# Kernel optimization log

Measured on AMD Instinct MI355X. Metric: run time of the kernel, lower is better.

Reference implementation:

```python
import jax, jax.numpy as jnp
import numpy as np

WS = 8          # window size
DISP = 4        # ws // 2 cyclic shift displacement
WS2 = WS * WS   # tokens per window
HEADS = 3
HD = 32         # head dim
SCALE = HD ** -0.5


def _mask(upper_lower, left_right):
    m = np.zeros((WS2, WS2), np.float32)
    if upper_lower:
        m[-DISP * WS:, :-DISP * WS] = -np.inf
        m[:-DISP * WS, -DISP * WS:] = -np.inf
    if left_right:
        m = m.reshape(WS, WS, WS, WS)
        m[:, -DISP:, :, :-DISP] = -np.inf
        m[:, :-DISP, :, -DISP:] = -np.inf
        m = m.reshape(WS2, WS2)
    return m

UL = _mask(True, False)
LR = _mask(False, True)
_ix = np.array([(i, j) for i in range(WS) for j in range(WS)])
REL = (_ix[None] - _ix[:, None]) + WS - 1  # [WS2, WS2, 2] relative index table


def _ln(x, g, b):
    m = x.mean(-1, keepdims=True)
    v = ((x - m) ** 2).mean(-1, keepdims=True)
    return (x - m) * jax.lax.rsqrt(v + 1e-5) * g + b


def _wattn(x, Wqkv, pos, Wo, bo, shifted):
    if shifted:
        x = jnp.roll(x, (-DISP, -DISP), axis=(1, 2))
    b, H, W, _ = x.shape
    nh, nw = H // WS, W // WS
    # qkv: last dim laid out as (3, heads, head_dim) matching torch chunk + rearrange
    qkv = (x @ Wqkv).reshape(b, nh, WS, nw, WS, 3, HEADS, HD)
    qkv = qkv.transpose(5, 0, 6, 1, 3, 2, 4, 7).reshape(3, b, HEADS, nh * nw, WS2, HD)
    q, k, v = qkv[0], qkv[1], qkv[2]
    dots = jnp.einsum('bhwid,bhwjd->bhwij', q, k) * SCALE  # [b,h,nwin,ws2,ws2]
    dots = dots + pos[REL[..., 0], REL[..., 1]]            # relative pos bias
    if shifted:
        m = np.zeros((nh * nw, WS2, WS2), np.float32)
        m[-nw:] += UL             # windows in last row
        m[nw - 1::nw] += LR       # windows in last column
        dots = dots + jnp.asarray(m)[None, None]
    a = jax.nn.softmax(dots, axis=-1)
    o = jnp.einsum('bhwij,bhwjd->bhwid', a, v)
    o = o.reshape(b, HEADS, nh, nw, WS, WS, HD).transpose(0, 2, 4, 3, 5, 1, 6).reshape(b, H, W, HEADS * HD)
    o = o @ Wo + bo
    if shifted:
        o = jnp.roll(o, (DISP, DISP), axis=(1, 2))
    return o


def _block(t, g1, b1, Wqkv, pos, Wo, bo, g2, b2, W1, bf1, W2, bf2, shifted):
    t = t + _wattn(_ln(t, g1, b1), Wqkv, pos, Wo, bo, shifted)
    h = _ln(t, g2, b2)
    return t + (jax.nn.gelu(h @ W1 + bf1, approximate=False) @ W2 + bf2)


def _stage(x, Wm, bm, pa, pb):
    b, c, H, W = x.shape
    nh, nw = H // 2, W // 2
    # PatchMerging: Unfold(k=2,s=2) layout is (c, ki, kj) with c outermost
    t = x.reshape(b, c, nh, 2, nw, 2).transpose(0, 2, 4, 1, 3, 5).reshape(b, nh, nw, c * 4)
    t = t @ Wm + bm
    t = _block(t, *pa, False)
    t = _block(t, *pb, True)
    return t.transpose(0, 3, 1, 2)


def setup_inputs() -> dict:
    key = jax.random.key(0)
    ks = jax.random.split(key, 12)
    def w(k, shp):
        return jax.random.normal(k, shp, jnp.float32) * 0.02
    def blk(kw, kp, ko, k1, k2):
        return {'g1': jnp.ones((128,), jnp.float32), 'b1': jnp.zeros((128,), jnp.float32),
                'Wqkv': w(kw, (128, 288)), 'pos': jax.random.normal(kp, (15, 15), jnp.float32),
                'Wo': w(ko, (96, 128)), 'bo': jnp.zeros((128,), jnp.float32),
                'g2': jnp.ones((128,), jnp.float32), 'b2': jnp.zeros((128,), jnp.float32),
                'W1': w(k1, (128, 512)), 'bf1': jnp.zeros((512,), jnp.float32),
                'W2': w(k2, (512, 128)), 'bf2': jnp.zeros((128,), jnp.float32)}
    A = blk(ks[2], ks[3], ks[4], ks[5], ks[6])
    B = blk(ks[7], ks[8], ks[9], ks[10], ks[11])
    inp = {'x': jax.random.normal(ks[0], (8, 64, 256, 256), jnp.float32),
           'Wm': w(ks[1], (256, 128)), 'bm': jnp.zeros((128,), jnp.float32)}
    for n, v in A.items():
        inp[n + 'a'] = v
    for n, v in B.items():
        inp[n + 'b'] = v
    return inp


def reference(x, Wm, bm, g1a, b1a, Wqkva, posa, Woa, boa, g2a, b2a, W1a, bf1a, W2a, bf2a,
              g1b, b1b, Wqkvb, posb, Wob, bob, g2b, b2b, W1b, bf1b, W2b, bf2b):
    pa = (g1a, b1a, Wqkva, posa, Woa, boa, g2a, b2a, W1a, bf1a, W2a, bf2a)
    pb = (g1b, b1b, Wqkvb, posb, Wob, bob, g2b, b2b, W1b, bf1b, W2b, bf2b)
    return _stage(x, Wm, bm, pa, pb)
```

## Files before the change

kernel.cpp:

```cpp
#include <hip/hip_runtime.h>
#include <hip/hip_bf16.h>
#include <math.h>

#define Timg 131072
#define SCALE 0.17677669529663689f

typedef __attribute__((ext_vector_type(8))) short frag8;
typedef __attribute__((ext_vector_type(8))) unsigned short us8;
typedef __attribute__((ext_vector_type(4))) float f32x4;
typedef __attribute__((ext_vector_type(4))) unsigned int u32x4;

__device__ inline float bf2f(unsigned short u) {
    union { unsigned int i; float f; } v; v.i = ((unsigned int)u) << 16; return v.f;
}
__device__ inline unsigned short f2bf(float f) {
    __hip_bfloat16 h = __float2bfloat16(f);
    return *reinterpret_cast<unsigned short*>(&h);
}
__device__ inline unsigned int pk2(float lo, float hi) {
    return ((unsigned int)f2bf(hi) << 16) | (unsigned int)f2bf(lo);
}
__device__ inline float gelu_f(float x) {
    float u = x * x;
    float z = x * fmaf(u, 0.044715f, 1.0f);
    float e = __builtin_amdgcn_exp2f(-2.3025851f * z);
    return x * __builtin_amdgcn_rcpf(1.f + e);
}

__global__ __launch_bounds__(256) void k_wcvt(
    const float* __restrict__ src, unsigned short* __restrict__ dst, int R, int C,
    int qrows, float s)
{
    int idx = blockIdx.x * 256 + threadIdx.x;
    if (idx >= R * C) return;
    int r = idx / C, c = idx % C;
    float v = src[idx];
    if (c < qrows) v *= s;
    dst[(size_t)c * R + r] = f2bf(v);
}

#define LDA_PM 264
__global__ __launch_bounds__(256) void k_patchmerge(
    const float* __restrict__ x, const unsigned short* __restrict__ Wmt,
    const float* __restrict__ bm, float* __restrict__ t)
{
    __shared__ unsigned short A[64 * LDA_PM];
    int blk = blockIdx.x;
    int b   = blk >> 8;
    int rem = blk & 255;
    int h   = rem >> 1;
    int w0  = (rem & 1) * 64;
    int tid = threadIdx.x;
    {
        int row = tid >> 1, half = tid & 1;
        int c = row >> 1, ki = row & 1;
        const float* src = x + (((size_t)(b*64 + c))*256 + (size_t)(2*h + ki))*256 + 2*w0 + half*64;
        int base = c*4 + ki*2;
        #pragma unroll
        for (int q = 0; q < 16; ++q) {
            float4 v = *reinterpret_cast<const float4*>(src + q*4);
            int tk0 = (half*64 + q*4) >> 1;
            *reinterpret_cast<unsigned int*>(&A[ tk0     * LDA_PM + base]) = pk2(v.x, v.y);
            *reinterpret_cast<unsigned int*>(&A[(tk0 + 1)* LDA_PM + base]) = pk2(v.z, v.w);
        }
    }
    __syncthreads();
    int lane = tid & 63, w = tid >> 6;
    int lr = lane & 15, lg = lane >> 4;
    size_t tok0 = (size_t)blk * 64;
    #pragma unroll
    for (int nt = 0; nt < 2; ++nt) {
        int n0 = (w*2 + nt) * 16;
        f32x4 acc[4] = {};
        #pragma unroll
        for (int ks = 0; ks < 8; ++ks) {
            frag8 bfr = *reinterpret_cast<const frag8*>(Wmt + (size_t)(n0 + lr)*256 + ks*32 + lg*8);
            #pragma unroll
            for (int m = 0; m < 4; ++m) {
                frag8 af = *reinterpret_cast<const frag8*>(&A[(m*16 + lr)*LDA_PM + ks*32 + lg*8]);
                acc[m] = __builtin_amdgcn_mfma_f32_16x16x32_bf16(af, bfr, acc[m], 0, 0, 0);
            }
        }
        #pragma unroll
        for (int m = 0; m < 4; ++m)
            #pragma unroll
            for (int r = 0; r < 4; ++r) {
                int rowl = m*16 + lg*4 + r;
                int col  = n0 + lr;
                t[(tok0 + rowl)*128 + col] = acc[m][r] + bm[col];
            }
    }
}

#define LDQK 200
#define LDVT 72
#define LDP  72
#define LDAO 104
#define LDA  136
#define LDH  136
#define OFF_VT  25600
#define OFF_HC1 17408
#define R1SZ    39424
#define OFF_AO  48640
#define SMEMSZ  61952
__global__ __launch_bounds__(256, 2) void k_block(
    const float* __restrict__ pos, float* __restrict__ t,
    const float* __restrict__ g1, const float* __restrict__ b1,
    const unsigned short* __restrict__ Wqt,
    const unsigned short* __restrict__ Wot, const float* __restrict__ bo,
    const float* __restrict__ g2, const float* __restrict__ b2,
    const unsigned short* __restrict__ W1t, const float* __restrict__ bf1,
    const unsigned short* __restrict__ W2t, const float* __restrict__ bf2,
    int shifted)
{
    __shared__ __attribute__((aligned(16))) char smem[SMEMSZ];
    __shared__ float stats[64][4][2];
    __shared__ float ps[225];
    unsigned short* QK   = (unsigned short*)(smem);
    unsigned short* Vt   = (unsigned short*)(smem + OFF_VT);
    unsigned short* Hc0  = (unsigned short*)(smem);
    unsigned short* Hc1  = (unsigned short*)(smem + OFF_HC1);
    unsigned short* Abuf = (unsigned short*)(smem + R1SZ);
    unsigned short* P    = (unsigned short*)(smem + R1SZ);
    unsigned short* ao   = (unsigned short*)(smem + OFF_AO);

    int blk = blockIdx.x;
    int b   = blk >> 8;
    int win = blk & 255;
    int wy  = win >> 4, wx = win & 15;
    int tid = threadIdx.x, lane = tid & 63, w = tid >> 6;
    int lr  = lane & 15, lg = lane >> 4;
    int l16 = lane & 15, quad = lane >> 4;
    int sh  = shifted ? 4 : 0;

    for (int idx = tid; idx < 225; idx += 256) ps[idx] = pos[idx];

    float4 gv0 = *reinterpret_cast<const float4*>(g1 + l16*8);
    float4 gv1 = *reinterpret_cast<const float4*>(g1 + l16*8 + 4);
    float4 bv0 = *reinterpret_cast<const float4*>(b1 + l16*8);
    float4 bv1 = *reinterpret_cast<const float4*>(b1 + l16*8 + 4);
    #pragma unroll
    for (int it2 = 0; it2 < 4; ++it2) {
        int m  = w*16 + it2*4 + quad;
        int ir = m >> 3, ic = m & 7;
        int hh = (wy*8 + ir + sh) & 127, ww = (wx*8 + ic + sh) & 127;
        const float* p = t + ((size_t)((b*128 + hh)*128 + ww))*128 + l16*8;
        float4 v0 = *reinterpret_cast<const float4*>(p);
        float4 v1 = *reinterpret_cast<const float4*>(p + 4);
        float s = v0.x+v0.y+v0.z+v0.w + v1.x+v1.y+v1.z+v1.w;
        float q = v0.x*v0.x+v0.y*v0.y+v0.z*v0.z+v0.w*v0.w
                + v1.x*v1.x+v1.y*v1.y+v1.z*v1.z+v1.w*v1.w;
        #pragma unroll
        for (int o = 8; o; o >>= 1) { s += __shfl_xor(s, o); q += __shfl_xor(q, o); }
        float mean = s * 0.0078125f;
        float var  = fmaxf(q * 0.0078125f - mean*mean, 0.f);
        float rs   = rsqrtf(var + 1e-5f);
        u32x4 pk;
        pk.x = pk2((v0.x-mean)*rs*gv0.x + bv0.x, (v0.y-mean)*rs*gv0.y + bv0.y);
        pk.y = pk2((v0.z-mean)*rs*gv0.z + bv0.z, (v0.w-mean)*rs*gv0.w + bv0.w);
        pk.z = pk2((v1.x-mean)*rs*gv1.x + bv1.x, (v1.y-mean)*rs*gv1.y + bv1.y);
        pk.w = pk2((v1.z-mean)*rs*gv1.z + bv1.z, (v1.w-mean)*rs*gv1.w + bv1.w);
        *reinterpret_cast<u32x4*>(&Abuf[m*LDA + l16*8]) = pk;
    }
    __syncthreads();

    for (int nt = w; nt < 18; nt += 4) {
        f32x4 acc[4] = {};
        #pragma unroll
        for (int ks = 0; ks < 4; ++ks) {
            frag8 bfr = *reinterpret_cast<const frag8*>(Wqt + (size_t)(nt*16 + lr)*128 + ks*32 + lg*8);
            #pragma unroll
            for (int m = 0; m < 4; ++m) {
                frag8 af = *reinterpret_cast<const frag8*>(&Abuf[(m*16 + lr)*LDA + ks*32 + lg*8]);
                acc[m] = __builtin_amdgcn_mfma_f32_16x16x32_bf16(af, bfr, acc[m], 0, 0, 0);
            }
        }
        if (nt < 12) {
            #pragma unroll
            for (int m = 0; m < 4; ++m)
                #pragma unroll
                for (int r = 0; r < 4; ++r)
                    QK[(m*16 + lg*4 + r)*LDQK + nt*16 + lr] = f2bf(acc[m][r]);
        } else {
            #pragma unroll
            for (int m = 0; m < 4; ++m)
                #pragma unroll
                for (int r = 0; r < 4; ++r)
                    Vt[((nt - 12)*16 + lr)*LDVT + (m*16 + lg*4 + r)] = f2bf(acc[m][r]);
        }
    }
    __syncthreads();

    bool mUL = (shifted != 0) && (wy == 15);
    bool mLR = (shifted != 0) && (wx == 15);
    #pragma unroll 1
    for (int h = 0; h < 3; ++h) {
        frag8 qf = *reinterpret_cast<const frag8*>(&QK[(w*16 + lr)*LDQK + h*32 + lg*8]);
        f32x4 s[4];
        #pragma unroll
        for (int jt = 0; jt < 4; ++jt) {
            frag8 kf = *reinterpret_cast<const frag8*>(&QK[(jt*16 + lr)*LDQK + 96 + h*32 + lg*8]);
            f32x4 z = {0.f, 0.f, 0.f, 0.f};
            s[jt] = __builtin_amdgcn_mfma_f32_16x16x32_bf16(qf, kf, z, 0, 0, 0);
        }
        #pragma unroll
        for (int r = 0; r < 4; ++r) {
            int i  = w*16 + lg*4 + r;
            int ir = i >> 3, ic = i & 7;
            int ro = (7 - ir)*15 + (7 - ic);
            float vals[4]; float mx = -1e30f;
            #pragma unroll
            for (int jt = 0; jt < 4; ++jt) {
                int j = jt*16 + lr, jr = j >> 3, jc = j & 7;
                float val = s[jt][r] + ps[ro + jr*15 + jc];
                if ((mUL && ((jr >= 4) != (ir >= 4))) || (mLR && ((jc >= 4) != (ic >= 4)))) val = -1e30f;
                vals[jt] = val; mx = fmaxf(mx, val);
            }
            #pragma unroll
            for (int o = 8; o; o >>= 1) mx = fmaxf(mx, __shfl_xor(mx, o));
            float sum = 0.f;
            #pragma unroll
            for (int jt = 0; jt < 4; ++jt) { vals[jt] = __expf(vals[jt] - mx); sum += vals[jt]; }
            #pragma unroll
            for (int o = 8; o; o >>= 1) sum += __shfl_xor(sum, o);
            float inv = __builtin_amdgcn_rcpf(sum);
            #pragma unroll
            for (int jt = 0; jt < 4; ++jt)
                P[i*LDP + jt*16 + lr] = f2bf(vals[jt] * inv);
        }
        #pragma unroll
        for (int nd = 0; nd < 2; ++nd) {
            f32x4 o4 = {0.f, 0.f, 0.f, 0.f};
            #pragma unroll
            for (int kt = 0; kt < 2; ++kt) {
                frag8 pf = *reinterpret_cast<const frag8*>(&P[(w*16 + lr)*LDP + kt*32 + lg*8]);
                frag8 vf = *reinterpret_cast<const frag8*>(&Vt[(h*32 + nd*16 + lr)*LDVT + kt*32 + lg*8]);
                o4 = __builtin_amdgcn_mfma_f32_16x16x32_bf16(pf, vf, o4, 0, 0, 0);
            }
            #pragma unroll
            for (int r = 0; r < 4; ++r)
                ao[(w*16 + lg*4 + r)*LDAO + h*32 + nd*16 + lr] = f2bf(o4[r]);
        }
    }
    __syncthreads();

    f32x4 pacc[2][4] = {};
    #pragma unroll
    for (int ks = 0; ks < 3; ++ks) {
        frag8 bw0 = *reinterpret_cast<const frag8*>(Wot + (size_t)(w*32      + lr)*96 + ks*32 + lg*8);
        frag8 bw1 = *reinterpret_cast<const frag8*>(Wot + (size_t)(w*32 + 16 + lr)*96 + ks*32 + lg*8);
        #pragma unroll
        for (int m = 0; m < 4; ++m) {
            frag8 af = *reinterpret_cast<const frag8*>(&ao[(m*16 + lr)*LDAO + ks*32 + lg*8]);
            pacc[0][m] = __builtin_amdgcn_mfma_f32_16x16x32_bf16(af, bw0, pacc[0][m], 0, 0, 0);
            pacc[1][m] = __builtin_amdgcn_mfma_f32_16x16x32_bf16(af, bw1, pacc[1][m], 0, 0, 0);
        }
    }
    float t1[2][4][4];
    int   toks[4][4];
    #pragma unroll
    for (int m = 0; m < 4; ++m)
        #pragma unroll
        for (int r = 0; r < 4; ++r) {
            int rowl = m*16 + lg*4 + r;
            int ir = rowl >> 3, ic = rowl & 7;
            int hh = (wy*8 + ir + sh) & 127, ww = (wx*8 + ic + sh) & 127;
            toks[m][r] = (b*128 + hh)*128 + ww;
            #pragma unroll
            for (int nt = 0; nt < 2; ++nt) {
                int col = w*32 + nt*16 + lr;
                t1[nt][m][r] = t[(size_t)toks[m][r]*128 + col] + pacc[nt][m][r] + bo[col];
            }
        }
    #pragma unroll
    for (int m = 0; m < 4; ++m)
        #pragma unroll
        for (int r = 0; r < 4; ++r) {
            float v0 = t1[0][m][r], v1 = t1[1][m][r];
            float s = v0 + v1, q = v0*v0 + v1*v1;
            #pragma unroll
            for (int o = 8; o; o >>= 1) { s += __shfl_xor(s, o); q += __shfl_xor(q, o); }
            if (lr == 0) {
                int rowl = m*16 + lg*4 + r;
                stats[rowl][w][0] = s;
                stats[rowl][w][1] = q;
            }
        }
    __syncthreads();
    #pragma unroll
    for (int m = 0; m < 4; ++m)
        #pragma unroll
        for (int r = 0; r < 4; ++r) {
            int rowl = m*16 + lg*4 + r;
            float s = 0.f, q = 0.f;
            #pragma unroll
            for (int ww2 = 0; ww2 < 4; ++ww2) { s += stats[rowl][ww2][0]; q += stats[rowl][ww2][1]; }
            float mean = s * 0.0078125f;
            float var  = fmaxf(q * 0.0078125f - mean*mean, 0.f);
            float rs   = rsqrtf(var + 1e-5f);
            #pragma unroll
            for (int nt = 0; nt < 2; ++nt) {
                int col = w*32 + nt*16 + lr;
                Abuf[rowl*LDA + col] = f2bf((t1[nt][m][r] - mean)*rs*g2[col] + b2[col]);
            }
        }
    __syncthreads();

    f32x4 acc2[2][4] = {};
    #pragma unroll 1
    for (int kc = 0; kc < 4; ++kc) {
        unsigned short* Hc = (kc & 1) ? Hc1 : Hc0;
        f32x4 a1[2][4] = {};
        #pragma unroll
        for (int ks = 0; ks < 4; ++ks) {
            frag8 af[4];
            #pragma unroll
            for (int m = 0; m < 4; ++m)
                af[m] = *reinterpret_cast<const frag8*>(&Abuf[(m*16 + lr)*LDA + ks*32 + lg*8]);
            #pragma unroll
            for (int nt = 0; nt < 2; ++nt) {
                int n0 = kc*128 + w*32 + nt*16;
                frag8 bfr = *reinterpret_cast<const frag8*>(W1t + (size_t)(n0 + lr)*128 + ks*32 + lg*8);
                #pragma unroll
                for (int m = 0; m < 4; ++m)
                    a1[nt][m] = __builtin_amdgcn_mfma_f32_16x16x32_bf16(af[m], bfr, a1[nt][m], 0, 0, 0);
            }
        }
        #pragma unroll
        for (int nt = 0; nt < 2; ++nt)
            #pragma unroll
            for (int m = 0; m < 4; ++m)
                #pragma unroll
                for (int r = 0; r < 4; ++r) {
                    int rowl = m*16 + lg*4 + r;
                    int col  = w*32 + nt*16 + lr;
                    float xv = a1[nt][m][r] + bf1[kc*128 + col];
                    Hc[rowl*LDH + col] = f2bf(gelu_f(xv));
                }
        __syncthreads();
        #pragma unroll
        for (int ks = 0; ks < 4; ++ks) {
            frag8 hfk[4];
            #pragma unroll
            for (int m = 0; m < 4; ++m)
                hfk[m] = *reinterpret_cast<const frag8*>(&Hc[(m*16 + lr)*LDH + ks*32 + lg*8]);
            #pragma unroll
            for (int nt = 0; nt < 2; ++nt) {
                frag8 bfr = *reinterpret_cast<const frag8*>(W2t + (size_t)(w*32 + nt*16 + lr)*512 + kc*128 + ks*32 + lg*8);
                #pragma unroll
                for (int m = 0; m < 4; ++m)
                    acc2[nt][m] = __builtin_amdgcn_mfma_f32_16x16x32_bf16(hfk[m], bfr, acc2[nt][m], 0, 0, 0);
            }
        }
    }
    #pragma unroll
    for (int nt = 0; nt < 2; ++nt) {
        float bfv = bf2[w*32 + nt*16 + lr];
        #pragma unroll
        for (int m = 0; m < 4; ++m)
            #pragma unroll
            for (int r = 0; r < 4; ++r)
                t[(size_t)toks[m][r]*128 + w*32 + nt*16 + lr] = t1[nt][m][r] + acc2[nt][m][r] + bfv;
    }
}

__global__ __launch_bounds__(256) void k_transpose(
    const float* __restrict__ t, float* __restrict__ out)
{
    __shared__ float tile[128][33];
    int blk = blockIdx.x;
    int ct = blk & 3;
    int h  = (blk >> 2) & 127;
    int b  = blk >> 9;
    const float* src = t + ((size_t)b*16384 + (size_t)h*128)*128 + ct*32;
    #pragma unroll
    for (int q = 0; q < 16; ++q) {
        int idx = threadIdx.x + q*256;
        int w = idx >> 5, c = idx & 31;
        tile[w][c] = src[(size_t)w*128 + c];
    }
    __syncthreads();
    float* dst = out + ((size_t)(b*128 + ct*32))*16384 + (size_t)h*128;
    #pragma unroll
    for (int q = 0; q < 16; ++q) {
        int idx = threadIdx.x + q*256;
        int c = idx >> 7, w = idx & 127;
        dst[(size_t)c*16384 + w] = tile[w][c];
    }
}

extern "C" void kernel_launch(void* const* d_in, const int* in_sizes, int n_in,
                              void* d_out, int out_size, void* d_ws, size_t ws_size,
                              hipStream_t stream)
{
    const float* x  = (const float*)d_in[0];
    const float* Wm = (const float*)d_in[1];
    const float* bm = (const float*)d_in[2];

    float* t           = (float*)d_ws;
    unsigned short* wb = (unsigned short*)(t + (size_t)Timg*128);

    unsigned short* Wmt = wb;
    unsigned short* Wqt[2], *Wot[2], *W1t[2], *W2t[2];
    unsigned short* p = wb + 32768;
    for (int i = 0; i < 2; ++i) {
        Wqt[i] = p; p += 36864;
        Wot[i] = p; p += 12288;
        W1t[i] = p; p += 65536;
        W2t[i] = p; p += 65536;
    }

    k_wcvt<<<(256*128 + 255)/256, 256, 0, stream>>>(Wm, Wmt, 256, 128, 0, 1.f);
    for (int i = 0; i < 2; ++i) {
        k_wcvt<<<(128*288 + 255)/256, 256, 0, stream>>>((const float*)d_in[ 5 + i*12], Wqt[i], 128, 288, 96, SCALE);
        k_wcvt<<<( 96*128 + 255)/256, 256, 0, stream>>>((const float*)d_in[ 7 + i*12], Wot[i],  96, 128, 0, 1.f);
        k_wcvt<<<(128*512 + 255)/256, 256, 0, stream>>>((const float*)d_in[11 + i*12], W1t[i], 128, 512, 0, 1.f);
        k_wcvt<<<(512*128 + 255)/256, 256, 0, stream>>>((const float*)d_in[13 + i*12], W2t[i], 512, 128, 0, 1.f);
    }

    k_patchmerge<<<Timg/64, 256, 0, stream>>>(x, Wmt, bm, t);

    for (int blk = 0; blk < 2; ++blk) {
        const float* g1  = (const float*)d_in[ 3 + blk*12];
        const float* b1  = (const float*)d_in[ 4 + blk*12];
        const float* pos = (const float*)d_in[ 6 + blk*12];
        const float* bo  = (const float*)d_in[ 8 + blk*12];
        const float* g2  = (const float*)d_in[ 9 + blk*12];
        const float* b2  = (const float*)d_in[10 + blk*12];
        const float* bf1 = (const float*)d_in[12 + blk*12];
        const float* bf2 = (const float*)d_in[14 + blk*12];

        k_block<<<2048, 256, 0, stream>>>(pos, t, g1, b1, Wqt[blk],
                                          Wot[blk], bo, g2, b2,
                                          W1t[blk], bf1, W2t[blk], bf2, blk);
    }

    k_transpose<<<8*128*4, 256, 0, stream>>>(t, (float*)d_out);
}
```

Measured before the change: 383.1 us.

## Batch weight conversions into one launch, prefetch residual, add MFMA priority hints

Merges the nine per-weight conversion launches into a single 2D-grid kernel, so the host issues one launch instead of nine. In the block kernel, the residual values of t are loaded at the start, so their global-load latency overlaps the LayerNorm and QKV work, rather than being read after the output projection. It also wraps the MFMA loops in s_setprio(1)/s_setprio(0) so waves doing matrix math get scheduling priority. The early load keeps 32 more floats live per thread across the kernel, which raises register pressure and may lower occupancy.

Result: faster. 361.7 us (-5.6%).

```diff
diff --git a/kernel.cpp b/kernel.cpp
--- a/kernel.cpp
+++ b/kernel.cpp
@@ -6,7 +6,6 @@
 #define SCALE 0.17677669529663689f
 
 typedef __attribute__((ext_vector_type(8))) short frag8;
-typedef __attribute__((ext_vector_type(8))) unsigned short us8;
 typedef __attribute__((ext_vector_type(4))) float f32x4;
 typedef __attribute__((ext_vector_type(4))) unsigned int u32x4;
 
@@ -27,16 +26,23 @@
     return x * __builtin_amdgcn_rcpf(1.f + e);
 }
 
-__global__ __launch_bounds__(256) void k_wcvt(
-    const float* __restrict__ src, unsigned short* __restrict__ dst, int R, int C,
-    int qrows, float s)
+struct WcvtAll {
+    const float* src[9];
+    unsigned short* dst[9];
+    int R[9];
+    int C[9];
+    int qrows[9];
+};
+__global__ __launch_bounds__(256) void k_wcvt_all(WcvtAll wa, float s)
 {
+    int wsel = blockIdx.y;
+    int R = wa.R[wsel], C = wa.C[wsel];
     int idx = blockIdx.x * 256 + threadIdx.x;
     if (idx >= R * C) return;
     int r = idx / C, c = idx % C;
-    float v = src[idx];
-    if (c < qrows) v *= s;
-    dst[(size_t)c * R + r] = f2bf(v);
+    float v = wa.src[wsel][idx];
+    if (c < wa.qrows[wsel]) v *= s;
+    wa.dst[wsel][(size_t)c * R + r] = f2bf(v);
 }
 
 #define LDA_PM 264
@@ -135,6 +141,21 @@
 
     for (int idx = tid; idx < 225; idx += 256) ps[idx] = pos[idx];
 
+    int   toks[4][4];
+    float t1raw[2][4][4];
+    #pragma unroll
+    for (int m = 0; m < 4; ++m)
+        #pragma unroll
+        for (int r = 0; r < 4; ++r) {
+            int rowl = m*16 + lg*4 + r;
+            int ir = rowl >> 3, ic = rowl & 7;
+            int hh = (wy*8 + ir + sh) & 127, ww = (wx*8 + ic + sh) & 127;
+            toks[m][r] = (b*128 + hh)*128 + ww;
+            #pragma unroll
+            for (int nt = 0; nt < 2; ++nt)
+                t1raw[nt][m][r] = t[(size_t)toks[m][r]*128 + w*32 + nt*16 + lr];
+        }
+
     float4 gv0 = *reinterpret_cast<const float4*>(g1 + l16*8);
     float4 gv1 = *reinterpret_cast<const float4*>(g1 + l16*8 + 4);
     float4 bv0 = *reinterpret_cast<const float4*>(b1 + l16*8);
@@ -164,6 +185,7 @@
     }
     __syncthreads();
 
+    __builtin_amdgcn_s_setprio(1);
     for (int nt = w; nt < 18; nt += 4) {
         f32x4 acc[4] = {};
         #pragma unroll
@@ -189,6 +211,7 @@
                     Vt[((nt - 12)*16 + lr)*LDVT + (m*16 + lg*4 + r)] = f2bf(acc[m][r]);
         }
     }
+    __builtin_amdgcn_s_setprio(0);
     __syncthreads();
 
     bool mUL = (shifted != 0) && (wy == 15);
@@ -257,21 +280,15 @@
         }
     }
     float t1[2][4][4];
-    int   toks[4][4];
-    #pragma unroll
-    for (int m = 0; m < 4; ++m)
-        #pragma unroll
-        for (int r = 0; r < 4; ++r) {
-            int rowl = m*16 + lg*4 + r;
-            int ir = rowl >> 3, ic = rowl & 7;
-            int hh = (wy*8 + ir + sh) & 127, ww = (wx*8 + ic + sh) & 127;
-            toks[m][r] = (b*128 + hh)*128 + ww;
-            #pragma unroll
-            for (int nt = 0; nt < 2; ++nt) {
-                int col = w*32 + nt*16 + lr;
-                t1[nt][m][r] = t[(size_t)toks[m][r]*128 + col] + pacc[nt][m][r] + bo[col];
-            }
-        }
+    #pragma unroll
+    for (int nt = 0; nt < 2; ++nt) {
+        float bov = bo[w*32 + nt*16 + lr];
+        #pragma unroll
+        for (int m = 0; m < 4; ++m)
+            #pragma unroll
+            for (int r = 0; r < 4; ++r)
+                t1[nt][m][r] = t1raw[nt][m][r] + pacc[nt][m][r] + bov;
+    }
     #pragma unroll
     for (int m = 0; m < 4; ++m)
         #pragma unroll
@@ -311,6 +328,7 @@
     for (int kc = 0; kc < 4; ++kc) {
         unsigned short* Hc = (kc & 1) ? Hc1 : Hc0;
         f32x4 a1[2][4] = {};
+        __builtin_amdgcn_s_setprio(1);
         #pragma unroll
         for (int ks = 0; ks < 4; ++ks) {
             frag8 af[4];
@@ -326,6 +344,7 @@
                     a1[nt][m] = __builtin_amdgcn_mfma_f32_16x16x32_bf16(af[m], bfr, a1[nt][m], 0, 0, 0);
             }
         }
+        __builtin_amdgcn_s_setprio(0);
         #pragma unroll
         for (int nt = 0; nt < 2; ++nt)
             #pragma unroll
@@ -338,6 +357,7 @@
                     Hc[rowl*LDH + col] = f2bf(gelu_f(xv));
                 }
         __syncthreads();
+        __builtin_amdgcn_s_setprio(1);
         #pragma unroll
         for (int ks = 0; ks < 4; ++ks) {
             frag8 hfk[4];
@@ -352,6 +372,7 @@
                     acc2[nt][m] = __builtin_amdgcn_mfma_f32_16x16x32_bf16(hfk[m], bfr, acc2[nt][m], 0, 0, 0);
             }
         }
+        __builtin_amdgcn_s_setprio(0);
     }
     #pragma unroll
     for (int nt = 0; nt < 2; ++nt) {
@@ -410,13 +431,19 @@
         W2t[i] = p; p += 65536;
     }
 
-    k_wcvt<<<(256*128 + 255)/256, 256, 0, stream>>>(Wm, Wmt, 256, 128, 0, 1.f);
+    WcvtAll wa;
+    int slot = 0;
+    auto put = [&](const float* s, unsigned short* d, int R, int C, int q) {
+        wa.src[slot] = s; wa.dst[slot] = d; wa.R[slot] = R; wa.C[slot] = C; wa.qrows[slot] = q; ++slot;
+    };
+    put(Wm, Wmt, 256, 128, 0);
     for (int i = 0; i < 2; ++i) {
-        k_wcvt<<<(128*288 + 255)/256, 256, 0, stream>>>((const float*)d_in[ 5 + i*12], Wqt[i], 128, 288, 96, SCALE);
-        k_wcvt<<<( 96*128 + 255)/256, 256, 0, stream>>>((const float*)d_in[ 7 + i*12], Wot[i],  96, 128, 0, 1.f);
-        k_wcvt<<<(128*512 + 255)/256, 256, 0, stream>>>((const float*)d_in[11 + i*12], W1t[i], 128, 512, 0, 1.f);
-        k_wcvt<<<(512*128 + 255)/256, 256, 0, stream>>>((const float*)d_in[13 + i*12], W2t[i], 512, 128, 0, 1.f);
-    }
+        put((const float*)d_in[ 5 + i*12], Wqt[i], 128, 288, 96);
+        put((const float*)d_in[ 7 + i*12], Wot[i],  96, 128, 0);
+        put((const float*)d_in[11 + i*12], W1t[i], 128, 512, 0);
+        put((const float*)d_in[13 + i*12], W2t[i], 512, 128, 0);
+    }
+    k_wcvt_all<<<dim3(256, 9), 256, 0, stream>>>(wa, SCALE);
 
     k_patchmerge<<<Timg/64, 256, 0, stream>>>(x, Wmt, bm, t);
 
```
